# Optimization experiments

Hardware: AMD Instinct MI355X
Metric: run time of the kernel (lower is better)

The kernel has to match this reference:

```python
import jax, jax.numpy as jnp
import numpy as np

B, N, D, H = 4, 2048, 512, 8
HD = D // H


def setup_inputs() -> dict:
    key = jax.random.key(0)
    ks = jax.random.split(key, 12)
    s = 1.0 / np.sqrt(D)
    return {
        "node_feat": jax.random.normal(ks[0], (B, N, D), jnp.float32),
        "edge_weights": jax.random.uniform(ks[1], (B, N, N), jnp.float32),
        "adj_matrix": jax.random.uniform(ks[2], (B, N, N), jnp.float32),
        "masks": jnp.ones((B, N), jnp.float32),
        "class_token": 0.02 * jax.random.normal(ks[3], (1, 1, D), jnp.float32),
        "Wq": jax.random.uniform(ks[4], (D, D), jnp.float32, -s, s),
        "bq": jnp.zeros((D,), jnp.float32),
        "Wk": jax.random.uniform(ks[5], (D, D), jnp.float32, -s, s),
        "bk": jnp.zeros((D,), jnp.float32),
        "Wv": jax.random.uniform(ks[6], (D, D), jnp.float32, -s, s),
        "bv": jnp.zeros((D,), jnp.float32),
        "Wo": jax.random.uniform(ks[7], (D, D), jnp.float32, -s, s),
        "bo": jnp.zeros((D,), jnp.float32),
        "gamma": jnp.ones((D,), jnp.float32),
        "beta": jnp.zeros((D,), jnp.float32),
    }


def _attn_mask(edge_weights, masks):
    # inner block: edge gates + self-loops, clamped at 1
    inner = jnp.minimum(edge_weights + jnp.eye(N, dtype=edge_weights.dtype), 1.0)
    top = jnp.concatenate([jnp.ones((B, 1, 1), edge_weights.dtype), masks[:, None, :]], axis=2)  # [B,1,1+N]
    bot = jnp.concatenate([jnp.ones((B, N, 1), edge_weights.dtype), inner], axis=2)              # [B,N,1+N]
    m = jnp.concatenate([top, bot], axis=1)  # [B,1+N,1+N]
    ext = jnp.concatenate([jnp.ones((B, 1), masks.dtype), masks], axis=1)  # [B,1+N], CLS always valid
    return m * ext[:, None, :] * ext[:, :, None]


def reference(node_feat, edge_weights, adj_matrix, masks, class_token,
              Wq, bq, Wk, bk, Wv, bv, Wo, bo, gamma, beta):
    x = jnp.concatenate([jnp.broadcast_to(class_token, (B, 1, D)), node_feat], axis=1)  # [B,1+N,D]
    S = 1 + N
    q = (x @ Wq.T + bq).reshape(B, S, H, HD).transpose(0, 2, 1, 3)
    k = (x @ Wk.T + bk).reshape(B, S, H, HD).transpose(0, 2, 1, 3)
    v = (x @ Wv.T + bv).reshape(B, S, H, HD).transpose(0, 2, 1, 3)
    scores = jnp.einsum('bhqd,bhkd->bhqk', q, k) / jnp.sqrt(jnp.float32(HD))
    m = _attn_mask(edge_weights, masks)
    scores = jnp.where(m[:, None, :, :] == 0, jnp.float32(-1e9), scores)
    attn = jax.nn.softmax(scores, axis=-1)
    out = jnp.einsum('bhqk,bhkd->bhqd', attn, v).transpose(0, 2, 1, 3).reshape(B, S, D)
    out = out @ Wo.T + bo
    y = out + x
    mu = jnp.mean(y, axis=-1, keepdims=True)
    var = jnp.mean((y - mu) ** 2, axis=-1, keepdims=True)
    y = (y - mu) / jnp.sqrt(var + 1e-5) * gamma + beta
    return y[:, 0, :]
```

## Files before the change

### kernel.cpp

```cpp
#include <hip/hip_runtime.h>

#define B_ 4
#define N_ 2048
#define D_ 512
#define H_ 8
#define S_ (N_ + 1)
#define SCHUNK 64
#define NCHUNK ((S_ + SCHUNK - 1) / SCHUNK)

#define TQ_OFF   0
#define ATTN_OFF 8192
#define PW_OFF   81920
#define W_OFF    (PW_OFF + NCHUNK * B_ * H_ * D_)
#define O0_OFF   (W_OFF + B_ * H_ * D_)
#define Y_OFF    (O0_OFF + B_ * D_)

__device__ __forceinline__ float wave_reduce_sum(float v) {
    #pragma unroll
    for (int off = 32; off > 0; off >>= 1) v += __shfl_down(v, off, 64);
    return v;
}

__global__ void tq_kernel(const float* __restrict__ ct,
                          const float* __restrict__ Wq, const float* __restrict__ bq,
                          const float* __restrict__ Wk, float* __restrict__ ws) {
    int h = blockIdx.x, jc = blockIdx.y;
    int tid = threadIdx.x, wv = tid >> 6, lane = tid & 63;
    __shared__ float ct_sh[D_];
    __shared__ float q0_sh[64];
    ct_sh[tid] = ct[tid];
    ct_sh[tid + 256] = ct[tid + 256];
    __syncthreads();
    const float4* c4 = (const float4*)ct_sh;
    float4 ca = c4[lane * 2], cb = c4[lane * 2 + 1];
    #pragma unroll 1
    for (int rr = 0; rr < 16; ++rr) {
        int rl = wv * 16 + rr;
        int r = h * 64 + rl;
        const float4* row = (const float4*)(Wq + (size_t)r * D_);
        float4 a = row[lane * 2], b = row[lane * 2 + 1];
        float acc = a.x*ca.x + a.y*ca.y + a.z*ca.z + a.w*ca.w
                  + b.x*cb.x + b.y*cb.y + b.z*cb.z + b.w*cb.w;
        acc = wave_reduce_sum(acc);
        if (lane == 0) q0_sh[rl] = acc + bq[r];
    }
    __syncthreads();
    int j = jc * 256 + tid;
    float acc = 0.f;
    #pragma unroll 4
    for (int d2 = 0; d2 < 64; ++d2)
        acc += q0_sh[d2] * Wk[(size_t)(h * 64 + d2) * D_ + j];
    ws[TQ_OFF + h * D_ + j] = acc;
}

__global__ void scores_kernel(const float* __restrict__ nf, const float* __restrict__ ct,
                              const float* __restrict__ masks, float* __restrict__ ws) {
    int b = blockIdx.y;
    int wv = threadIdx.x >> 6, lane = threadIdx.x & 63;
    int s = blockIdx.x * 4 + wv;
    if (s >= S_) return;
    const float* xrow = (s == 0) ? ct : (nf + ((size_t)b * N_ + (s - 1)) * D_);
    const float4* x4 = (const float4*)xrow;
    float4 xa = x4[lane];
    float4 xb = x4[64 + lane];
    bool masked = (s > 0) && (masks[b * N_ + (s - 1)] == 0.0f);
    const float* tq = ws + TQ_OFF;
    #pragma unroll
    for (int h = 0; h < H_; ++h) {
        const float4* t4 = (const float4*)(tq + h * D_);
        float4 ta = t4[lane], tb = t4[64 + lane];
        float acc = ta.x*xa.x + ta.y*xa.y + ta.z*xa.z + ta.w*xa.w
                  + tb.x*xb.x + tb.y*xb.y + tb.z*xb.z + tb.w*xb.w;
        acc = wave_reduce_sum(acc);
        if (lane == 0) {
            float sc = acc * 0.125f;
            if (masked) sc = -1e9f;
            ws[ATTN_OFF + (size_t)(b * H_ + h) * S_ + s] = sc;
        }
    }
}

__global__ void softmax_kernel(float* __restrict__ ws) {
    int bh = blockIdx.x;
    float* sc = ws + ATTN_OFF + (size_t)bh * S_;
    int tid = threadIdx.x, wv = tid >> 6, lane = tid & 63;
    __shared__ float red[4];
    float m = -3e38f;
    for (int i = tid; i < S_; i += 256) m = fmaxf(m, sc[i]);
    #pragma unroll
    for (int off = 32; off > 0; off >>= 1) m = fmaxf(m, __shfl_down(m, off, 64));
    if (lane == 0) red[wv] = m;
    __syncthreads();
    m = fmaxf(fmaxf(red[0], red[1]), fmaxf(red[2], red[3]));
    __syncthreads();
    float sum = 0.f;
    for (int i = tid; i < S_; i += 256) { float e = __expf(sc[i] - m); sc[i] = e; sum += e; }
    sum = wave_reduce_sum(sum);
    if (lane == 0) red[wv] = sum;
    __syncthreads();
    float inv = 1.0f / (red[0] + red[1] + red[2] + red[3]);
    for (int i = tid; i < S_; i += 256) sc[i] *= inv;
}

__global__ void wsum_kernel(const float* __restrict__ nf, const float* __restrict__ ct,
                            float* __restrict__ ws) {
    int chunk = blockIdx.x;
    int b = blockIdx.y;
    int tid = threadIdx.x;
    __shared__ float sa[H_][SCHUNK];
    int s0 = chunk * SCHUNK;
    for (int idx = tid; idx < H_ * SCHUNK; idx += 128) {
        int h = idx >> 6, ss = idx & 63;
        int s = s0 + ss;
        sa[h][ss] = (s < S_) ? ws[ATTN_OFF + (size_t)(b * H_ + h) * S_ + s] : 0.f;
    }
    __syncthreads();
    float4 acc[H_];
    #pragma unroll
    for (int h = 0; h < H_; ++h) acc[h] = make_float4(0.f, 0.f, 0.f, 0.f);
    int smax = min(SCHUNK, S_ - s0);
    for (int ss = 0; ss < smax; ++ss) {
        int s = s0 + ss;
        const float* xrow = (s == 0) ? ct : (nf + ((size_t)b * N_ + (s - 1)) * D_);
        float4 xv = ((const float4*)xrow)[tid];
        #pragma unroll
        for (int h = 0; h < H_; ++h) {
            float a = sa[h][ss];
            acc[h].x += a * xv.x; acc[h].y += a * xv.y;
            acc[h].z += a * xv.z; acc[h].w += a * xv.w;
        }
    }
    float4* pw = (float4*)(ws + PW_OFF + (size_t)chunk * (B_ * H_ * D_) + (size_t)(b * H_) * D_);
    #pragma unroll
    for (int h = 0; h < H_; ++h)
        pw[h * (D_ / 4) + tid] = acc[h];
}

__global__ void reduce_w_kernel(float* __restrict__ ws) {
    int idx = blockIdx.x * 256 + threadIdx.x;
    float4 acc = make_float4(0.f, 0.f, 0.f, 0.f);
    #pragma unroll 1
    for (int c = 0; c < NCHUNK; ++c) {
        float4 v = ((const float4*)(ws + PW_OFF + (size_t)c * (B_ * H_ * D_)))[idx];
        acc.x += v.x; acc.y += v.y; acc.z += v.z; acc.w += v.w;
    }
    ((float4*)(ws + W_OFF))[idx] = acc;
}

__global__ void wv_kernel(const float* __restrict__ Wv, const float* __restrict__ bv,
                          float* __restrict__ ws) {
    int b = blockIdx.x;
    int wv = threadIdx.x >> 6, lane = threadIdx.x & 63;
    int r = blockIdx.y * 4 + wv;
    const float4* wrow = (const float4*)(ws + W_OFF + (size_t)b * H_ * D_ + (size_t)(r >> 6) * D_);
    float4 wa = wrow[lane * 2], wb = wrow[lane * 2 + 1];
    const float4* row = (const float4*)(Wv + (size_t)r * D_);
    float4 a = row[lane * 2], c = row[lane * 2 + 1];
    float acc = a.x*wa.x + a.y*wa.y + a.z*wa.z + a.w*wa.w
              + c.x*wb.x + c.y*wb.y + c.z*wb.z + c.w*wb.w;
    acc = wave_reduce_sum(acc);
    if (lane == 0) ws[O0_OFF + b * D_ + r] = acc + bv[r];
}

__global__ void wo_kernel(const float* __restrict__ Wo, const float* __restrict__ bo,
                          const float* __restrict__ ct, float* __restrict__ ws) {
    int b = blockIdx.x;
    int wv = threadIdx.x >> 6, lane = threadIdx.x & 63;
    int r = blockIdx.y * 4 + wv;
    const float4* ov = (const float4*)(ws + O0_OFF + (size_t)b * D_);
    float4 oa = ov[lane * 2], ob = ov[lane * 2 + 1];
    const float4* row = (const float4*)(Wo + (size_t)r * D_);
    float4 a = row[lane * 2], c = row[lane * 2 + 1];
    float acc = a.x*oa.x + a.y*oa.y + a.z*oa.z + a.w*oa.w
              + c.x*ob.x + c.y*ob.y + c.z*ob.z + c.w*ob.w;
    acc = wave_reduce_sum(acc);
    if (lane == 0) ws[Y_OFF + b * D_ + r] = acc + bo[r] + ct[r];
}

__global__ void ln_kernel(const float* __restrict__ gamma, const float* __restrict__ beta,
                          const float* __restrict__ ws, float* __restrict__ out) {
    int b = blockIdx.x;
    int tid = threadIdx.x, wv = tid >> 6, lane = tid & 63;
    float v = ws[Y_OFF + b * D_ + tid];
    float s1 = v, s2 = v * v;
    #pragma unroll
    for (int off = 32; off > 0; off >>= 1) {
        s1 += __shfl_down(s1, off, 64);
        s2 += __shfl_down(s2, off, 64);
    }
    __shared__ float r1[8], r2[8];
    if (lane == 0) { r1[wv] = s1; r2[wv] = s2; }
    __syncthreads();
    if (tid == 0) {
        float a = 0.f, c = 0.f;
        for (int i = 0; i < 8; ++i) { a += r1[i]; c += r2[i]; }
        r1[0] = a; r2[0] = c;
    }
    __syncthreads();
    float mean = r1[0] * (1.0f / D_);
    float var  = r2[0] * (1.0f / D_) - mean * mean;
    float rinv = rsqrtf(var + 1e-5f);
    out[b * D_ + tid] = (v - mean) * rinv * gamma[tid] + beta[tid];
}

extern "C" void kernel_launch(void* const* d_in, const int* in_sizes, int n_in,
                              void* d_out, int out_size, void* d_ws, size_t ws_size,
                              hipStream_t stream) {
    const float* nf    = (const float*)d_in[0];
    const float* masks = (const float*)d_in[3];
    const float* ct    = (const float*)d_in[4];
    const float* Wq    = (const float*)d_in[5];
    const float* bq    = (const float*)d_in[6];
    const float* Wk    = (const float*)d_in[7];
    const float* Wv    = (const float*)d_in[9];
    const float* bv    = (const float*)d_in[10];
    const float* Wo    = (const float*)d_in[11];
    const float* bo    = (const float*)d_in[12];
    const float* gamma = (const float*)d_in[13];
    const float* beta  = (const float*)d_in[14];
    float* ws  = (float*)d_ws;
    float* out = (float*)d_out;

    hipLaunchKernelGGL(tq_kernel, dim3(H_, 2), dim3(256), 0, stream,
                       ct, Wq, bq, Wk, ws);
    hipLaunchKernelGGL(scores_kernel, dim3((S_ + 3) / 4, B_), dim3(256), 0, stream,
                       nf, ct, masks, ws);
    hipLaunchKernelGGL(softmax_kernel, dim3(B_ * H_), dim3(256), 0, stream, ws);
    hipLaunchKernelGGL(wsum_kernel, dim3(NCHUNK, B_), dim3(128), 0, stream,
                       nf, ct, ws);
    hipLaunchKernelGGL(reduce_w_kernel, dim3(16), dim3(256), 0, stream, ws);
    hipLaunchKernelGGL(wv_kernel, dim3(B_, 128), dim3(256), 0, stream, Wv, bv, ws);
    hipLaunchKernelGGL(wo_kernel, dim3(B_, 128), dim3(256), 0, stream, Wo, bo, ct, ws);
    hipLaunchKernelGGL(ln_kernel, dim3(B_), dim3(512), 0, stream, gamma, beta, ws, out);
}
```

Baseline: 232.0 us.

## Fuse scores, softmax and weighted sum into a single pass over node features

Replaces the separate scores, softmax and weighted-sum kernels with one fused kernel. Each wave computes its rows' CLS-query scores, exponentiates them unnormalized, and accumulates both the partial value sums and the partial normalizers per slot. The reduce kernel then combines the slots and divides by the total normalizer, so node features are read once and two launches plus the score round-trip through memory disappear. The Wq projection is also split into its own more parallel kernel ahead of the Wk projection. The exponent no longer subtracts the row maximum, which risks overflow for large scores, and the fused grid has far fewer blocks than the old scores kernel.

```diff
diff --git a/kernel.cpp b/kernel.cpp
--- a/kernel.cpp
+++ b/kernel.cpp
@@ -5,146 +5,140 @@
 #define D_ 512
 #define H_ 8
 #define S_ (N_ + 1)
-#define SCHUNK 64
-#define NCHUNK ((S_ + SCHUNK - 1) / SCHUNK)
-
-#define TQ_OFF   0
-#define ATTN_OFF 8192
-#define PW_OFF   81920
-#define W_OFF    (PW_OFF + NCHUNK * B_ * H_ * D_)
-#define O0_OFF   (W_OFF + B_ * H_ * D_)
-#define Y_OFF    (O0_OFF + B_ * D_)
+#define NSLOT 132
+
+#define Q0_OFF 0
+#define TQ_OFF 1024
+#define PW_OFF 8192
+#define PZ_OFF (PW_OFF + NSLOT * B_ * H_ * D_)
+#define W_OFF  (PZ_OFF + NSLOT * B_ * H_)
+#define O0_OFF (W_OFF + B_ * H_ * D_)
+#define Y_OFF  (O0_OFF + B_ * D_)
 
 __device__ __forceinline__ float wave_reduce_sum(float v) {
     #pragma unroll
     for (int off = 32; off > 0; off >>= 1) v += __shfl_down(v, off, 64);
     return v;
 }
-
-__global__ void tq_kernel(const float* __restrict__ ct,
+__device__ __forceinline__ float wave_allreduce_sum(float v) {
+    #pragma unroll
+    for (int off = 1; off < 64; off <<= 1) v += __shfl_xor(v, off, 64);
+    return v;
+}
+
+__global__ void q0_kernel(const float* __restrict__ ct,
                           const float* __restrict__ Wq, const float* __restrict__ bq,
-                          const float* __restrict__ Wk, float* __restrict__ ws) {
+                          float* __restrict__ ws) {
+    int wv = threadIdx.x >> 6, lane = threadIdx.x & 63;
+    int r = blockIdx.x * 8 + wv;
+    const float4* c4 = (const float4*)ct;
+    float4 ca = c4[lane * 2], cb = c4[lane * 2 + 1];
+    const float4* row = (const float4*)(Wq + (size_t)r * D_);
+    float4 a = row[lane * 2], b = row[lane * 2 + 1];
+    float acc = a.x*ca.x + a.y*ca.y + a.z*ca.z + a.w*ca.w
+              + b.x*cb.x + b.y*cb.y + b.z*cb.z + b.w*cb.w;
+    acc = wave_reduce_sum(acc);
+    if (lane == 0) ws[Q0_OFF + r] = acc + bq[r];
+}
+
+__global__ void tq_kernel(const float* __restrict__ Wk, float* __restrict__ ws) {
     int h = blockIdx.x, jc = blockIdx.y;
-    int tid = threadIdx.x, wv = tid >> 6, lane = tid & 63;
-    __shared__ float ct_sh[D_];
-    __shared__ float q0_sh[64];
-    ct_sh[tid] = ct[tid];
-    ct_sh[tid + 256] = ct[tid + 256];
-    __syncthreads();
-    const float4* c4 = (const float4*)ct_sh;
-    float4 ca = c4[lane * 2], cb = c4[lane * 2 + 1];
-    #pragma unroll 1
-    for (int rr = 0; rr < 16; ++rr) {
-        int rl = wv * 16 + rr;
-        int r = h * 64 + rl;
-        const float4* row = (const float4*)(Wq + (size_t)r * D_);
-        float4 a = row[lane * 2], b = row[lane * 2 + 1];
-        float acc = a.x*ca.x + a.y*ca.y + a.z*ca.z + a.w*ca.w
-                  + b.x*cb.x + b.y*cb.y + b.z*cb.z + b.w*cb.w;
-        acc = wave_reduce_sum(acc);
-        if (lane == 0) q0_sh[rl] = acc + bq[r];
-    }
-    __syncthreads();
-    int j = jc * 256 + tid;
+    int tid = threadIdx.x;
+    __shared__ float q0s[64];
+    if (tid < 64) q0s[tid] = ws[Q0_OFF + h * 64 + tid];
+    __syncthreads();
+    int j = jc * 128 + tid;
     float acc = 0.f;
-    #pragma unroll 4
+    #pragma unroll 8
     for (int d2 = 0; d2 < 64; ++d2)
-        acc += q0_sh[d2] * Wk[(size_t)(h * 64 + d2) * D_ + j];
+        acc += q0s[d2] * Wk[(size_t)(h * 64 + d2) * D_ + j];
     ws[TQ_OFF + h * D_ + j] = acc;
 }
 
-__global__ void scores_kernel(const float* __restrict__ nf, const float* __restrict__ ct,
-                              const float* __restrict__ masks, float* __restrict__ ws) {
-    int b = blockIdx.y;
-    int wv = threadIdx.x >> 6, lane = threadIdx.x & 63;
-    int s = blockIdx.x * 4 + wv;
-    if (s >= S_) return;
-    const float* xrow = (s == 0) ? ct : (nf + ((size_t)b * N_ + (s - 1)) * D_);
-    const float4* x4 = (const float4*)xrow;
-    float4 xa = x4[lane];
-    float4 xb = x4[64 + lane];
-    bool masked = (s > 0) && (masks[b * N_ + (s - 1)] == 0.0f);
-    const float* tq = ws + TQ_OFF;
+__global__ void fused_kernel(const float* __restrict__ nf, const float* __restrict__ ct,
+                             const float* __restrict__ masks, float* __restrict__ ws) {
+    int chunk = blockIdx.x, b = blockIdx.y;
+    int wv = threadIdx.x >> 6, lane = threadIdx.x & 63;
+    int slot = chunk * 4 + wv;
+    int s0 = chunk * 64 + wv * 16;
+    const float4* tq4 = (const float4*)(ws + TQ_OFF);
+    float4 tqa[H_], tqb[H_];
     #pragma unroll
     for (int h = 0; h < H_; ++h) {
-        const float4* t4 = (const float4*)(tq + h * D_);
-        float4 ta = t4[lane], tb = t4[64 + lane];
-        float acc = ta.x*xa.x + ta.y*xa.y + ta.z*xa.z + ta.w*xa.w
-                  + tb.x*xb.x + tb.y*xb.y + tb.z*xb.z + tb.w*xb.w;
-        acc = wave_reduce_sum(acc);
-        if (lane == 0) {
-            float sc = acc * 0.125f;
-            if (masked) sc = -1e9f;
-            ws[ATTN_OFF + (size_t)(b * H_ + h) * S_ + s] = sc;
-        }
-    }
-}
-
-__global__ void softmax_kernel(float* __restrict__ ws) {
-    int bh = blockIdx.x;
-    float* sc = ws + ATTN_OFF + (size_t)bh * S_;
-    int tid = threadIdx.x, wv = tid >> 6, lane = tid & 63;
-    __shared__ float red[4];
-    float m = -3e38f;
-    for (int i = tid; i < S_; i += 256) m = fmaxf(m, sc[i]);
-    #pragma unroll
-    for (int off = 32; off > 0; off >>= 1) m = fmaxf(m, __shfl_down(m, off, 64));
-    if (lane == 0) red[wv] = m;
-    __syncthreads();
-    m = fmaxf(fmaxf(red[0], red[1]), fmaxf(red[2], red[3]));
-    __syncthreads();
-    float sum = 0.f;
-    for (int i = tid; i < S_; i += 256) { float e = __expf(sc[i] - m); sc[i] = e; sum += e; }
-    sum = wave_reduce_sum(sum);
-    if (lane == 0) red[wv] = sum;
-    __syncthreads();
-    float inv = 1.0f / (red[0] + red[1] + red[2] + red[3]);
-    for (int i = tid; i < S_; i += 256) sc[i] *= inv;
-}
-
-__global__ void wsum_kernel(const float* __restrict__ nf, const float* __restrict__ ct,
-                            float* __restrict__ ws) {
-    int chunk = blockIdx.x;
-    int b = blockIdx.y;
-    int tid = threadIdx.x;
-    __shared__ float sa[H_][SCHUNK];
-    int s0 = chunk * SCHUNK;
-    for (int idx = tid; idx < H_ * SCHUNK; idx += 128) {
-        int h = idx >> 6, ss = idx & 63;
-        int s = s0 + ss;
-        sa[h][ss] = (s < S_) ? ws[ATTN_OFF + (size_t)(b * H_ + h) * S_ + s] : 0.f;
-    }
-    __syncthreads();
-    float4 acc[H_];
-    #pragma unroll
-    for (int h = 0; h < H_; ++h) acc[h] = make_float4(0.f, 0.f, 0.f, 0.f);
-    int smax = min(SCHUNK, S_ - s0);
-    for (int ss = 0; ss < smax; ++ss) {
-        int s = s0 + ss;
-        const float* xrow = (s == 0) ? ct : (nf + ((size_t)b * N_ + (s - 1)) * D_);
-        float4 xv = ((const float4*)xrow)[tid];
+        tqa[h] = tq4[h * 128 + lane * 2];
+        tqb[h] = tq4[h * 128 + lane * 2 + 1];
+    }
+    float4 acca[H_], accb[H_];
+    float z[H_];
+    #pragma unroll
+    for (int h = 0; h < H_; ++h) {
+        acca[h] = make_float4(0.f, 0.f, 0.f, 0.f);
+        accb[h] = make_float4(0.f, 0.f, 0.f, 0.f);
+        z[h] = 0.f;
+    }
+    for (int i = 0; i < 16; ++i) {
+        int s = s0 + i;
+        bool valid = (s < S_);
+        const float* xrow = (!valid || s == 0) ? ct : (nf + ((size_t)b * N_ + (s - 1)) * D_);
+        const float4* x4 = (const float4*)xrow;
+        float4 xa = x4[lane * 2], xb = x4[lane * 2 + 1];
+        float msk = 1.0f;
+        if (valid && s > 0) msk = masks[b * N_ + s - 1];
+        float gate = (valid && msk != 0.0f) ? 1.0f : 0.0f;
+        float p[H_];
         #pragma unroll
         for (int h = 0; h < H_; ++h) {
-            float a = sa[h][ss];
-            acc[h].x += a * xv.x; acc[h].y += a * xv.y;
-            acc[h].z += a * xv.z; acc[h].w += a * xv.w;
+            p[h] = tqa[h].x*xa.x + tqa[h].y*xa.y + tqa[h].z*xa.z + tqa[h].w*xa.w
+                 + tqb[h].x*xb.x + tqb[h].y*xb.y + tqb[h].z*xb.z + tqb[h].w*xb.w;
+            p[h] = wave_allreduce_sum(p[h]);
         }
-    }
-    float4* pw = (float4*)(ws + PW_OFF + (size_t)chunk * (B_ * H_ * D_) + (size_t)(b * H_) * D_);
-    #pragma unroll
-    for (int h = 0; h < H_; ++h)
-        pw[h * (D_ / 4) + tid] = acc[h];
+        #pragma unroll
+        for (int h = 0; h < H_; ++h) {
+            float e = gate * __expf(p[h] * 0.125f);
+            z[h] += e;
+            acca[h].x += e * xa.x; acca[h].y += e * xa.y;
+            acca[h].z += e * xa.z; acca[h].w += e * xa.w;
+            accb[h].x += e * xb.x; accb[h].y += e * xb.y;
+            accb[h].z += e * xb.z; accb[h].w += e * xb.w;
+        }
+    }
+    float4* pw4 = (float4*)(ws + PW_OFF);
+    size_t base = ((size_t)slot * B_ + b) * H_;
+    #pragma unroll
+    for (int h = 0; h < H_; ++h) {
+        pw4[(base + h) * 128 + lane * 2]     = acca[h];
+        pw4[(base + h) * 128 + lane * 2 + 1] = accb[h];
+    }
+    if (lane == 0) {
+        #pragma unroll
+        for (int h = 0; h < H_; ++h)
+            ws[PZ_OFF + (slot * B_ + b) * H_ + h] = z[h];
+    }
 }
 
 __global__ void reduce_w_kernel(float* __restrict__ ws) {
-    int idx = blockIdx.x * 256 + threadIdx.x;
+    int b = blockIdx.x / H_, h = blockIdx.x % H_;
+    int tid = threadIdx.x;
+    __shared__ float zl[128];
+    float zp = 0.f;
+    for (int slot = tid; slot < NSLOT; slot += 128)
+        zp += ws[PZ_OFF + (slot * B_ + b) * H_ + h];
+    zl[tid] = zp;
+    __syncthreads();
+    for (int st = 64; st > 0; st >>= 1) {
+        if (tid < st) zl[tid] += zl[tid + st];
+        __syncthreads();
+    }
+    float zinv = 1.0f / zl[0];
+    const float4* pw4 = (const float4*)(ws + PW_OFF);
     float4 acc = make_float4(0.f, 0.f, 0.f, 0.f);
-    #pragma unroll 1
-    for (int c = 0; c < NCHUNK; ++c) {
-        float4 v = ((const float4*)(ws + PW_OFF + (size_t)c * (B_ * H_ * D_)))[idx];
+    #pragma unroll 4
+    for (int slot = 0; slot < NSLOT; ++slot) {
+        float4 v = pw4[(((size_t)slot * B_ + b) * H_ + h) * 128 + tid];
         acc.x += v.x; acc.y += v.y; acc.z += v.z; acc.w += v.w;
     }
-    ((float4*)(ws + W_OFF))[idx] = acc;
+    acc.x *= zinv; acc.y *= zinv; acc.z *= zinv; acc.w *= zinv;
+    ((float4*)(ws + W_OFF))[(b * H_ + h) * 128 + tid] = acc;
 }
 
 __global__ void wv_kernel(const float* __restrict__ Wv, const float* __restrict__ bv,
@@ -221,14 +215,10 @@
     float* ws  = (float*)d_ws;
     float* out = (float*)d_out;
 
-    hipLaunchKernelGGL(tq_kernel, dim3(H_, 2), dim3(256), 0, stream,
-                       ct, Wq, bq, Wk, ws);
-    hipLaunchKernelGGL(scores_kernel, dim3((S_ + 3) / 4, B_), dim3(256), 0, stream,
-                       nf, ct, masks, ws);
-    hipLaunchKernelGGL(softmax_kernel, dim3(B_ * H_), dim3(256), 0, stream, ws);
-    hipLaunchKernelGGL(wsum_kernel, dim3(NCHUNK, B_), dim3(128), 0, stream,
-                       nf, ct, ws);
-    hipLaunchKernelGGL(reduce_w_kernel, dim3(16), dim3(256), 0, stream, ws);
+    hipLaunchKernelGGL(q0_kernel, dim3(64), dim3(512), 0, stream, ct, Wq, bq, ws);
+    hipLaunchKernelGGL(tq_kernel, dim3(H_, 4), dim3(128), 0, stream, Wk, ws);
+    hipLaunchKernelGGL(fused_kernel, dim3(33, B_), dim3(256), 0, stream, nf, ct, masks, ws);
+    hipLaunchKernelGGL(reduce_w_kernel, dim3(B_ * H_), dim3(128), 0, stream, ws);
     hipLaunchKernelGGL(wv_kernel, dim3(B_, 128), dim3(256), 0, stream, Wv, bv, ws);
     hipLaunchKernelGGL(wo_kernel, dim3(B_, 128), dim3(256), 0, stream, Wo, bo, ct, ws);
     hipLaunchKernelGGL(ln_kernel, dim3(B_), dim3(512), 0, stream, gamma, beta, ws, out);
```

Result: no change. 233.5 us (+0.7%).
